# Optimization experiments

Measured on AMD Instinct MI355X. Metric: run time of the kernel, lower is better.

## Reference

```python
import jax, jax.numpy as jnp
import numpy as np

GRID_SIZE = 5   # efficient-kan default
ORDER = 3       # spline_order default


def make_grid(in_features):
    # extended grid on [-1, 1]: (in_features, GRID_SIZE + 2*ORDER + 1)
    h = 2.0 / GRID_SIZE
    g = jnp.arange(-ORDER, GRID_SIZE + ORDER + 1, dtype=jnp.float32) * h - 1.0
    return jnp.broadcast_to(g, (in_features, g.shape[0]))


def b_splines(x, grid):
    # x: (B, I), grid: (I, G) -> (B, I, GRID_SIZE + ORDER) via Cox-de Boor
    xg = x[..., None]
    bases = ((xg >= grid[:, :-1]) & (xg < grid[:, 1:])).astype(x.dtype)
    for k in range(1, ORDER + 1):
        left = (xg - grid[:, :-(k + 1)]) / (grid[:, k:-1] - grid[:, :-(k + 1)]) * bases[..., :-1]
        right = (grid[:, k + 1:] - xg) / (grid[:, k + 1:] - grid[:, 1:-k]) * bases[..., 1:]
        bases = left + right
    return bases


def kan_linear(x, base_w, spline_w, scaler, grid):
    # base path: silu(x) @ W_b^T ; spline path: bases contracted with scaled spline weight
    bases = b_splines(x, grid)                      # (B, I, C)
    sw = spline_w * scaler[..., None]               # (O, I, C)
    return jax.nn.silu(x) @ base_w.T + jnp.einsum('bic,oic->bo', bases, sw)


def setup_inputs() -> dict:
    key = jax.random.key(0)
    ks = jax.random.split(key, 9)
    B, I, H, O, E, C = 4096, 512, 512, 512, 8, GRID_SIZE + ORDER
    s = 0.1
    return {
        'x': jax.random.normal(ks[0], (B, I), jnp.float32),
        'gate_w': jax.random.normal(ks[1], (E, I), jnp.float32) * 0.02,
        'gate_b': jnp.zeros((E,), jnp.float32),
        'base_w1': jax.random.normal(ks[2], (E, H, I), jnp.float32) * s,
        'spline_w1': jax.random.normal(ks[3], (E, H, I, C), jnp.float32) * s,
        'scaler1': jax.random.normal(ks[4], (E, H, I), jnp.float32) * s + 1.0,
        'base_w2': jax.random.normal(ks[5], (E, O, H), jnp.float32) * s,
        'spline_w2': jax.random.normal(ks[6], (E, O, H, C), jnp.float32) * s,
        'scaler2': jax.random.normal(ks[7], (E, O, H), jnp.float32) * s + 1.0,
    }


def reference(x, gate_w, gate_b, base_w1, spline_w1, scaler1, base_w2, spline_w2, scaler2):
    gate_probs = jax.nn.softmax(x @ gate_w.T + gate_b, axis=-1)  # (B, E)
    grid1 = make_grid(x.shape[-1])
    grid2 = make_grid(base_w1.shape[1])

    def expert(bw1, sw1, sc1, bw2, sw2, sc2):
        h = kan_linear(x, bw1, sw1, sc1, grid1)      # (B, H)
        return kan_linear(h, bw2, sw2, sc2, grid2)   # (B, O)

    expert_outputs = jax.vmap(expert)(base_w1, spline_w1, scaler1,
                                      base_w2, spline_w2, scaler2)  # (E, B, O)
    return jnp.einsum('be,ebo->bo', gate_probs, expert_outputs)
```

## Files before the change

kernel.cpp:

```cpp
#include <hip/hip_runtime.h>

typedef __attribute__((ext_vector_type(4))) float f32x4;
typedef __attribute__((ext_vector_type(8))) _Float16 f16x8;

__device__ __forceinline__ void bspline8(float x, float b[8]) {
  float c[11];
#pragma unroll
  for (int j = 0; j < 11; ++j) {
    float t0 = (float)(j - 3) * 0.4f - 1.0f;
    float t1 = (float)(j - 2) * 0.4f - 1.0f;
    c[j] = (x >= t0 && x < t1) ? 1.0f : 0.0f;
  }
#pragma unroll
  for (int k = 1; k <= 3; ++k) {
#pragma unroll
    for (int j = 0; j + k < 11; ++j) {
      float tj   = (float)(j - 3) * 0.4f - 1.0f;
      float tjk  = (float)(j + k - 3) * 0.4f - 1.0f;
      float tj1  = (float)(j - 2) * 0.4f - 1.0f;
      float tjk1 = (float)(j + k - 2) * 0.4f - 1.0f;
      c[j] = (x - tj) * (1.0f / (tjk - tj)) * c[j] +
             (tjk1 - x) * (1.0f / (tjk1 - tj1)) * c[j + 1];
    }
  }
#pragma unroll
  for (int j = 0; j < 8; ++j) b[j] = c[j];
}

__global__ __launch_bounds__(256) void gate_kernel(const float* __restrict__ x,
                                                   const float* __restrict__ gw,
                                                   const float* __restrict__ gb,
                                                   float* __restrict__ gate) {
  const int b = blockIdx.x * 4 + (threadIdx.x >> 6);
  const int lane = threadIdx.x & 63;
  f32x4 x0 = *(const f32x4*)(x + ((size_t)b << 9) + lane * 8);
  f32x4 x1 = *(const f32x4*)(x + ((size_t)b << 9) + lane * 8 + 4);
  float lg[8];
#pragma unroll
  for (int e = 0; e < 8; ++e) {
    f32x4 w0 = *(const f32x4*)(gw + ((size_t)e << 9) + lane * 8);
    f32x4 w1 = *(const f32x4*)(gw + ((size_t)e << 9) + lane * 8 + 4);
    float d = 0.f;
#pragma unroll
    for (int j = 0; j < 4; ++j) d += x0[j] * w0[j] + x1[j] * w1[j];
#pragma unroll
    for (int m = 32; m >= 1; m >>= 1) d += __shfl_xor(d, m, 64);
    lg[e] = d + gb[e];
  }
  float mx = lg[0];
#pragma unroll
  for (int e = 1; e < 8; ++e) mx = fmaxf(mx, lg[e]);
  float p[8], ssum = 0.f;
#pragma unroll
  for (int e = 0; e < 8; ++e) { p[e] = __expf(lg[e] - mx); ssum += p[e]; }
  float mine = 0.f;
#pragma unroll
  for (int e = 0; e < 8; ++e) mine = (lane == e) ? p[e] / ssum : mine;
  if (lane < 8) gate[(size_t)b * 8 + lane] = mine;
}

__global__ __launch_bounds__(256) void prep_w_kernel(const float* __restrict__ bw,
                                                     const float* __restrict__ sw,
                                                     const float* __restrict__ sc,
                                                     _Float16* __restrict__ W) {
  size_t tid = (size_t)blockIdx.x * 256 + threadIdx.x;
  const size_t NSPL = (size_t)4096 * 512;
  if (tid < NSPL) {
    size_t row = tid >> 9;
    int i = (int)(tid & 511);
    float s = sc[(row << 9) + i];
    const float* sp = sw + (((row << 9) + (size_t)i) << 3);
    f32x4 v0 = *(const f32x4*)sp;
    f32x4 v1 = *(const f32x4*)(sp + 4);
    f16x8 o;
#pragma unroll
    for (int j = 0; j < 4; ++j) { o[j] = (_Float16)(v0[j] * s); o[4 + j] = (_Float16)(v1[j] * s); }
    *(f16x8*)(W + row * 4608 + 512 + (size_t)i * 8) = o;
  } else {
    size_t t2 = tid - NSPL;
    size_t row = t2 >> 6;
    int i8 = (int)((t2 & 63) << 3);
    const float* bp = bw + (row << 9) + i8;
    f32x4 v0 = *(const f32x4*)bp;
    f32x4 v1 = *(const f32x4*)(bp + 4);
    f16x8 o;
#pragma unroll
    for (int j = 0; j < 4; ++j) { o[j] = (_Float16)v0[j]; o[4 + j] = (_Float16)v1[j]; }
    *(f16x8*)(W + row * 4608 + i8) = o;
  }
}

__global__ __launch_bounds__(256) void expand_x_kernel(const float* __restrict__ x,
                                                       _Float16* __restrict__ A1, int chunk0) {
  const int tid = blockIdx.x * 256 + threadIdx.x;
  const int r = tid >> 9;
  const int i = tid & 511;
  const float xv = x[((size_t)(chunk0 + r) << 9) + i];
  const float s = xv / (1.0f + __expf(-xv));
  float bsv[8];
  bspline8(xv, bsv);
  _Float16* drow = A1 + (size_t)r * 4608;
  drow[i] = (_Float16)s;
  f16x8 v;
#pragma unroll
  for (int j = 0; j < 8; ++j) v[j] = (_Float16)bsv[j];
  *(f16x8*)(drow + 512 + (size_t)i * 8) = v;
}

template <int MODE>
__global__ __launch_bounds__(256) void kan_gemm(const _Float16* __restrict__ Abase,
                                                const _Float16* __restrict__ Wbase,
                                                _Float16* __restrict__ A2out,
                                                float* __restrict__ out_acc,
                                                const float* __restrict__ gate,
                                                int chunk0, int Mc) {
  __shared__ _Float16 As[128 * 32];
  __shared__ _Float16 Bs[128 * 32];
  const int t = threadIdx.x;
  const int z = blockIdx.z;
  const int tileM = blockIdx.x * 128;
  const int tileN = blockIdx.y * 128;

  const _Float16* A = (MODE == 1) ? Abase : (Abase + (size_t)z * Mc * 4608);
  const _Float16* B = Wbase + (size_t)z * 512 * 4608;

  const int srow = t >> 2;
  const int scol = (t & 3) * 8;
  const _Float16* gA0 = A + (size_t)(tileM + srow) * 4608 + scol;
  const _Float16* gA1 = A + (size_t)(tileM + 64 + srow) * 4608 + scol;
  const _Float16* gB0 = B + (size_t)(tileN + srow) * 4608 + scol;
  const _Float16* gB1 = B + (size_t)(tileN + 64 + srow) * 4608 + scol;
  _Float16* lA0 = &As[t * 8];
  _Float16* lA1 = &As[2048 + t * 8];
  _Float16* lB0 = &Bs[t * 8];
  _Float16* lB1 = &Bs[2048 + t * 8];

  const int lane = t & 63;
  const int wm = ((t >> 6) & 1) * 64;
  const int wn = ((t >> 6) >> 1) * 64;
  const int l16 = lane & 15;
  const int quad = lane >> 4;

  f32x4 acc[4][4];
#pragma unroll
  for (int i = 0; i < 4; ++i)
#pragma unroll
    for (int j = 0; j < 4; ++j) acc[i][j] = (f32x4){0.f, 0.f, 0.f, 0.f};

  for (int k0 = 0; k0 < 4608; k0 += 32) {
    f16x8 vA0 = *(const f16x8*)(gA0 + k0);
    f16x8 vA1 = *(const f16x8*)(gA1 + k0);
    f16x8 vB0 = *(const f16x8*)(gB0 + k0);
    f16x8 vB1 = *(const f16x8*)(gB1 + k0);
    *(f16x8*)lA0 = vA0;
    *(f16x8*)lA1 = vA1;
    *(f16x8*)lB0 = vB0;
    *(f16x8*)lB1 = vB1;
    __syncthreads();
    f16x8 af[4], bfr[4];
#pragma unroll
    for (int mt = 0; mt < 4; ++mt)
      af[mt] = *(const f16x8*)(&As[(wm + mt * 16 + l16) * 32 + quad * 8]);
#pragma unroll
    for (int nt = 0; nt < 4; ++nt)
      bfr[nt] = *(const f16x8*)(&Bs[(wn + nt * 16 + l16) * 32 + quad * 8]);
#pragma unroll
    for (int mt = 0; mt < 4; ++mt)
#pragma unroll
      for (int nt = 0; nt < 4; ++nt)
        acc[mt][nt] = __builtin_amdgcn_mfma_f32_16x16x32_f16(af[mt], bfr[nt], acc[mt][nt], 0, 0, 0);
    __syncthreads();
  }

  if (MODE == 1) {
    _Float16* dst = A2out + (size_t)z * Mc * 4608;
#pragma unroll
    for (int mt = 0; mt < 4; ++mt) {
#pragma unroll
      for (int r = 0; r < 4; ++r) {
        const int m = tileM + wm + mt * 16 + quad * 4 + r;
        _Float16* drow = dst + (size_t)m * 4608;
#pragma unroll
        for (int nt = 0; nt < 4; ++nt) {
          const int n = tileN + wn + nt * 16 + l16;
          const float h = acc[mt][nt][r];
          const float s = h / (1.0f + __expf(-h));
          float bsv[8];
          bspline8(h, bsv);
          drow[n] = (_Float16)s;
          f16x8 v;
#pragma unroll
          for (int j = 0; j < 8; ++j) v[j] = (_Float16)bsv[j];
          *(f16x8*)(drow + 512 + (size_t)n * 8) = v;
        }
      }
    }
  } else {
#pragma unroll
    for (int mt = 0; mt < 4; ++mt) {
#pragma unroll
      for (int r = 0; r < 4; ++r) {
        const int m = tileM + wm + mt * 16 + quad * 4 + r;
        const float gp = gate[(size_t)(chunk0 + m) * 8 + z];
        float* orow = out_acc + (size_t)(chunk0 + m) * 512;
#pragma unroll
        for (int nt = 0; nt < 4; ++nt) {
          const int n = tileN + wn + nt * 16 + l16;
          atomicAdd(orow + n, gp * acc[mt][nt][r]);
        }
      }
    }
  }
}

extern "C" void kernel_launch(void* const* d_in, const int* in_sizes, int n_in,
                              void* d_out, int out_size, void* d_ws, size_t ws_size,
                              hipStream_t stream) {
  (void)in_sizes; (void)n_in; (void)out_size;
  const float* x   = (const float*)d_in[0];
  const float* gw  = (const float*)d_in[1];
  const float* gb  = (const float*)d_in[2];
  const float* bw1 = (const float*)d_in[3];
  const float* sw1 = (const float*)d_in[4];
  const float* sc1 = (const float*)d_in[5];
  const float* bw2 = (const float*)d_in[6];
  const float* sw2 = (const float*)d_in[7];
  const float* sc2 = (const float*)d_in[8];
  float* out = (float*)d_out;

  const size_t GATE_B = (size_t)4096 * 8 * 4;
  const size_t W_B    = (size_t)8 * 512 * 4608 * 2;
  auto al = [](size_t v) { return (v + 255) & ~(size_t)255; };

  int Mc = 128;
  const int cand[6] = {4096, 2048, 1024, 512, 256, 128};
  const size_t fixedB = al(GATE_B) + 2 * al(W_B);
  for (int ci = 0; ci < 6; ++ci) {
    size_t need = fixedB + al((size_t)cand[ci] * 4608 * 2) + al((size_t)8 * cand[ci] * 4608 * 2);
    if (need <= ws_size) { Mc = cand[ci]; break; }
  }

  char* p = (char*)d_ws;
  float* gate      = (float*)p; p += al(GATE_B);
  _Float16* W1     = (_Float16*)p; p += al(W_B);
  _Float16* W2     = (_Float16*)p; p += al(W_B);
  _Float16* A1     = (_Float16*)p; p += al((size_t)Mc * 4608 * 2);
  _Float16* A2     = (_Float16*)p;

  hipMemsetAsync(out, 0, (size_t)4096 * 512 * 4, stream);
  gate_kernel<<<1024, 256, 0, stream>>>(x, gw, gb, gate);
  prep_w_kernel<<<9216, 256, 0, stream>>>(bw1, sw1, sc1, W1);
  prep_w_kernel<<<9216, 256, 0, stream>>>(bw2, sw2, sc2, W2);

  for (int c0 = 0; c0 < 4096; c0 += Mc) {
    expand_x_kernel<<<Mc * 2, 256, 0, stream>>>(x, A1, c0);
    dim3 grid(Mc / 128, 4, 8);
    kan_gemm<1><<<grid, 256, 0, stream>>>(A1, W1, A2, nullptr, nullptr, c0, Mc);
    kan_gemm<2><<<grid, 256, 0, stream>>>(A2, W2, nullptr, out, gate, c0, Mc);
  }
}
```

Baseline: 810.5 us.

## Use direct global-to-LDS async loads and split-K the second expert GEMM

The GEMM main loop now uses the global_load_lds builtin, so tiles go from global memory into shared memory without passing through registers. The second-layer GEMM is also split along K into two halves, which doubles its grid so more workgroups run at once. The two halves still combine through the existing atomicAdd into the output. This doubles the atomic traffic, and it relies on the async LDS load being complete at __syncthreads, which carries a correctness risk if the compiler does not insert the needed vmcnt waits.

```diff
diff --git a/kernel.cpp b/kernel.cpp
--- a/kernel.cpp
+++ b/kernel.cpp
@@ -2,6 +2,13 @@
 
 typedef __attribute__((ext_vector_type(4))) float f32x4;
 typedef __attribute__((ext_vector_type(8))) _Float16 f16x8;
+
+#define AS1 __attribute__((address_space(1)))
+#define AS3 __attribute__((address_space(3)))
+
+__device__ __forceinline__ void async16(const void* g, void* l) {
+  __builtin_amdgcn_global_load_lds((const AS1 void*)g, (AS3 void*)l, 16, 0, 0);
+}
 
 __device__ __forceinline__ void bspline8(float x, float b[8]) {
   float c[11];
@@ -118,11 +125,14 @@
   __shared__ _Float16 Bs[128 * 32];
   const int t = threadIdx.x;
   const int z = blockIdx.z;
+  const int e = (MODE == 1) ? z : (z >> 1);
+  const int kbeg = (MODE == 1) ? 0 : (z & 1) * 2304;
+  const int kend = (MODE == 1) ? 4608 : kbeg + 2304;
   const int tileM = blockIdx.x * 128;
   const int tileN = blockIdx.y * 128;
 
-  const _Float16* A = (MODE == 1) ? Abase : (Abase + (size_t)z * Mc * 4608);
-  const _Float16* B = Wbase + (size_t)z * 512 * 4608;
+  const _Float16* A = (MODE == 1) ? Abase : (Abase + (size_t)e * Mc * 4608);
+  const _Float16* B = Wbase + (size_t)e * 512 * 4608;
 
   const int srow = t >> 2;
   const int scol = (t & 3) * 8;
@@ -147,15 +157,11 @@
 #pragma unroll
     for (int j = 0; j < 4; ++j) acc[i][j] = (f32x4){0.f, 0.f, 0.f, 0.f};
 
-  for (int k0 = 0; k0 < 4608; k0 += 32) {
-    f16x8 vA0 = *(const f16x8*)(gA0 + k0);
-    f16x8 vA1 = *(const f16x8*)(gA1 + k0);
-    f16x8 vB0 = *(const f16x8*)(gB0 + k0);
-    f16x8 vB1 = *(const f16x8*)(gB1 + k0);
-    *(f16x8*)lA0 = vA0;
-    *(f16x8*)lA1 = vA1;
-    *(f16x8*)lB0 = vB0;
-    *(f16x8*)lB1 = vB1;
+  for (int k0 = kbeg; k0 < kend; k0 += 32) {
+    async16(gA0 + k0, lA0);
+    async16(gA1 + k0, lA1);
+    async16(gB0 + k0, lB0);
+    async16(gB1 + k0, lB1);
     __syncthreads();
     f16x8 af[4], bfr[4];
 #pragma unroll
@@ -173,7 +179,7 @@
   }
 
   if (MODE == 1) {
-    _Float16* dst = A2out + (size_t)z * Mc * 4608;
+    _Float16* dst = A2out + (size_t)e * Mc * 4608;
 #pragma unroll
     for (int mt = 0; mt < 4; ++mt) {
 #pragma unroll
@@ -201,7 +207,7 @@
 #pragma unroll
       for (int r = 0; r < 4; ++r) {
         const int m = tileM + wm + mt * 16 + quad * 4 + r;
-        const float gp = gate[(size_t)(chunk0 + m) * 8 + z];
+        const float gp = gate[(size_t)(chunk0 + m) * 8 + e];
         float* orow = out_acc + (size_t)(chunk0 + m) * 512;
 #pragma unroll
         for (int nt = 0; nt < 4; ++nt) {
@@ -254,8 +260,9 @@
 
   for (int c0 = 0; c0 < 4096; c0 += Mc) {
     expand_x_kernel<<<Mc * 2, 256, 0, stream>>>(x, A1, c0);
-    dim3 grid(Mc / 128, 4, 8);
-    kan_gemm<1><<<grid, 256, 0, stream>>>(A1, W1, A2, nullptr, nullptr, c0, Mc);
-    kan_gemm<2><<<grid, 256, 0, stream>>>(A2, W2, nullptr, out, gate, c0, Mc);
-  }
-}
+    dim3 grid1(Mc / 128, 4, 8);
+    dim3 grid2(Mc / 128, 4, 16);
+    kan_gemm<1><<<grid1, 256, 0, stream>>>(A1, W1, A2, nullptr, nullptr, c0, Mc);
+    kan_gemm<2><<<grid2, 256, 0, stream>>>(A2, W2, nullptr, out, gate, c0, Mc);
+  }
+}
```

After: 840.9 us. 3.8% more time.
